# Optimization experiments

Measured on AMD Instinct MI355X. Metric: run time of the kernel, lower is better.

The kernel has to match this reference:

```python
import jax, jax.numpy as jnp
import numpy as np

EMBED_DIM = 32
HIDDEN_DIM = 16

def _xavier(key, fan_in, fan_out):
    limit = float(np.sqrt(6.0 / (fan_in + fan_out)))
    return jax.random.uniform(key, (fan_in, fan_out), jnp.float32, -limit, limit)

def setup_inputs() -> dict:
    key = jax.random.key(0)
    ks = jax.random.split(key, 7)
    N = 1_000_000
    H = jax.random.normal(ks[0], (N, EMBED_DIM), jnp.float32)
    TPL = jax.random.normal(ks[1], (1, 1), jnp.float32)
    # params (xavier-uniform weights, zero biases, matching torch init)
    Wv = _xavier(ks[2], EMBED_DIM, HIDDEN_DIM); bv = jnp.zeros((HIDDEN_DIM,), jnp.float32)
    Wu = _xavier(ks[3], EMBED_DIM, HIDDEN_DIM); bu = jnp.zeros((HIDDEN_DIM,), jnp.float32)
    Ww = _xavier(ks[4], HIDDEN_DIM, 1);        bw = jnp.zeros((1,), jnp.float32)
    W1 = _xavier(ks[5], EMBED_DIM + 1, HIDDEN_DIM); b1 = jnp.zeros((HIDDEN_DIM,), jnp.float32)
    W2 = _xavier(ks[6], HIDDEN_DIM, 1);        b2 = jnp.zeros((1,), jnp.float32)
    return {"H": H, "TPL": TPL, "Wv": Wv, "bv": bv, "Wu": Wu, "bu": bu,
            "Ww": Ww, "bw": bw, "W1": W1, "b1": b1, "W2": W2, "b2": b2}

def reference(H, TPL, Wv, bv, Wu, bu, Ww, bw, W1, b1, W2, b2):
    # Gated attention: V (tanh branch) * U (sigmoid branch); dropout off (eval mode)
    V = jnp.tanh(H @ Wv + bv)                       # (N, hid)
    U = jax.nn.sigmoid(H @ Wu + bu)                 # (N, hid)
    G = V * U                                       # (N, hid)
    A_raw = G @ Ww + bw                             # (N, 1)
    alpha = jax.nn.softmax(A_raw.T, axis=1)         # (1, N)
    B = alpha @ H                                   # (1, D) attention-pooled bag rep
    B_fused = jnp.concatenate([B, TPL], axis=1)     # (1, D+1)
    h = jax.nn.relu(B_fused @ W1 + b1)              # (1, hid)
    score = h @ W2 + b2                             # (1, 1)
    return (score, alpha)
```

## Files before the change

kernel.cpp:

```cpp
#include <hip/hip_runtime.h>

#define NBLK   1024
#define TPB    256
#define D      32
#define HID    16
#define CHUNK  16
#define STRIDE 36
#define NWAVES (NBLK * 4)

__global__ __launch_bounds__(TPB, 4)
void k1_logits(const float* __restrict__ H,
               const float* __restrict__ Wv, const float* __restrict__ bv,
               const float* __restrict__ Wu, const float* __restrict__ bu,
               const float* __restrict__ Ww, const float* __restrict__ bw,
               float* __restrict__ eout,
               float* __restrict__ partials,
               int N)
{
    __shared__ float lds[TPB / 64][CHUNK * STRIDE];
    __shared__ float red[TPB / 64][D + 1];

    const int tid  = threadIdx.x;
    const int wave = tid >> 6;
    const int lane = tid & 63;
    const int g    = lane >> 4;
    const int h    = lane & 15;

    float wv[D], wu[D];
    #pragma unroll
    for (int d = 0; d < D; ++d) {
        wv[d] = Wv[d * HID + h];
        wu[d] = Wu[d * HID + h];
    }
    const float bvh = bv[h], buh = bu[h], wwh = Ww[h], bw0 = bw[0];

    float s_acc = 0.0f, vec0 = 0.0f, vec1 = 0.0f;

    float* slice = lds[wave];
    const int nchunk = N / CHUNK;
    int c = blockIdx.x * (TPB / 64) + wave;

    float4 pre0, pre1;
    bool has = (c < nchunk);
    if (has) {
        const float4* src = reinterpret_cast<const float4*>(H + (size_t)c * CHUNK * D);
        pre0 = src[lane];
        pre1 = src[lane + 64];
    }

    while (has) {
        {
            const int f0 = lane,      r0i = f0 >> 3, q0 = f0 & 7;
            const int f1 = lane + 64, r1i = f1 >> 3, q1 = f1 & 7;
            *reinterpret_cast<float4*>(&slice[r0i * STRIDE + q0 * 4]) = pre0;
            *reinterpret_cast<float4*>(&slice[r1i * STRIDE + q1 * 4]) = pre1;
        }

        const int cn = c + NWAVES;
        const bool hn = (cn < nchunk);
        if (hn) {
            const float4* src = reinterpret_cast<const float4*>(H + (size_t)cn * CHUNK * D);
            pre0 = src[lane];
            pre1 = src[lane + 64];
        }

        #pragma unroll
        for (int s = 0; s < 4; ++s) {
            const int rr = s * 4 + g;
            const float* row = &slice[rr * STRIDE];

            float v = bvh, u = buh;
            #pragma unroll
            for (int q = 0; q < 8; ++q) {
                const float4 t4 = *reinterpret_cast<const float4*>(&row[q * 4]);
                v = fmaf(t4.x, wv[q * 4 + 0], v);  u = fmaf(t4.x, wu[q * 4 + 0], u);
                v = fmaf(t4.y, wv[q * 4 + 1], v);  u = fmaf(t4.y, wu[q * 4 + 1], u);
                v = fmaf(t4.z, wv[q * 4 + 2], v);  u = fmaf(t4.z, wu[q * 4 + 2], u);
                v = fmaf(t4.w, wv[q * 4 + 3], v);  u = fmaf(t4.w, wu[q * 4 + 3], u);
            }
            const float th = 1.0f - 2.0f / (__expf(2.0f * v) + 1.0f);
            const float sg = 1.0f / (1.0f + __expf(-u));
            float pa = th * sg * wwh;
            pa += __shfl_xor(pa, 1);
            pa += __shfl_xor(pa, 2);
            pa += __shfl_xor(pa, 4);
            pa += __shfl_xor(pa, 8);
            const float e = __expf(pa + bw0);
            if (h == 0) eout[c * CHUNK + rr] = e;
            s_acc += e;
            const float2 rp = *reinterpret_cast<const float2*>(&row[2 * h]);
            vec0 = fmaf(e, rp.x, vec0);
            vec1 = fmaf(e, rp.y, vec1);
        }
        c = cn;
        has = hn;
    }

    s_acc += __shfl_xor(s_acc, 16);  s_acc += __shfl_xor(s_acc, 32);
    vec0  += __shfl_xor(vec0, 16);   vec0  += __shfl_xor(vec0, 32);
    vec1  += __shfl_xor(vec1, 16);   vec1  += __shfl_xor(vec1, 32);

    if (lane == 0) red[wave][0] = s_acc;
    if (lane < 16) {
        red[wave][1 + 2 * h] = vec0;
        red[wave][2 + 2 * h] = vec1;
    }
    __syncthreads();
    if (tid < D + 1) {
        float p = red[0][tid] + red[1][tid] + red[2][tid] + red[3][tid];
        partials[(size_t)tid * NBLK + blockIdx.x] = p;
    }
}

__global__ __launch_bounds__(320)
void k2_reduce(const float* __restrict__ partials,
               const float* __restrict__ TPL,
               const float* __restrict__ W1, const float* __restrict__ b1,
               const float* __restrict__ W2, const float* __restrict__ b2,
               float* __restrict__ score_out,
               float* __restrict__ scalars)
{
    __shared__ double red[D + 1][8];
    __shared__ double tot[D + 1];
    const int t = threadIdx.x;

    if (t < (D + 1) * 8) {
        const int j = t >> 3, sl = t & 7;
        double acc = 0.0;
        for (int b = sl; b < NBLK; b += 8)
            acc += (double)partials[(size_t)j * NBLK + b];
        red[j][sl] = acc;
    }
    __syncthreads();
    if (t < D + 1) {
        double a = 0.0;
        #pragma unroll
        for (int k = 0; k < 8; ++k) a += red[t][k];
        tot[t] = a;
    }
    __syncthreads();
    if (t < HID) {
        const double S = tot[0];
        float hj = b1[t];
        #pragma unroll
        for (int k = 0; k < D; ++k)
            hj = fmaf((float)(tot[1 + k] / S), W1[k * HID + t], hj);
        hj = fmaf(TPL[0], W1[D * HID + t], hj);
        hj = fmaxf(hj, 0.0f);
        float pre = hj * W2[t];
        pre += __shfl_xor(pre, 1);
        pre += __shfl_xor(pre, 2);
        pre += __shfl_xor(pre, 4);
        pre += __shfl_xor(pre, 8);
        if (t == 0) {
            score_out[0] = pre + b2[0];
            scalars[0] = (float)(1.0 / S);
        }
    }
}

__global__ __launch_bounds__(TPB)
void k3_alpha(float* __restrict__ alpha, const float* __restrict__ scalars, int N)
{
    const int i = blockIdx.x * TPB + threadIdx.x;
    if (i < N) alpha[i] = alpha[i] * scalars[0];
}

extern "C" void kernel_launch(void* const* d_in, const int* in_sizes, int n_in,
                              void* d_out, int out_size, void* d_ws, size_t ws_size,
                              hipStream_t stream) {
    const float* H   = (const float*)d_in[0];
    const float* TPL = (const float*)d_in[1];
    const float* Wv  = (const float*)d_in[2];
    const float* bv  = (const float*)d_in[3];
    const float* Wu  = (const float*)d_in[4];
    const float* bu  = (const float*)d_in[5];
    const float* Ww  = (const float*)d_in[6];
    const float* bw  = (const float*)d_in[7];
    const float* W1  = (const float*)d_in[8];
    const float* b1  = (const float*)d_in[9];
    const float* W2  = (const float*)d_in[10];
    const float* b2  = (const float*)d_in[11];

    float* out = (float*)d_out;
    const int N = in_sizes[0] / D;

    float* ws       = (float*)d_ws;
    float* partials = ws;
    float* scalars  = ws + (size_t)(D + 1) * NBLK;

    k1_logits<<<NBLK, TPB, 0, stream>>>(H, Wv, bv, Wu, bu, Ww, bw,
                                        out + 1, partials, N);
    k2_reduce<<<1, 320, 0, stream>>>(partials, TPL, W1, b1, W2, b2, out, scalars);
    k3_alpha<<<(N + TPB - 1) / TPB, TPB, 0, stream>>>(out + 1, scalars, N);
}
```

Measured before the change: 236.4 us.

## Parallelize partial reduction, vectorize alpha scaling, spread logit stores, hoist prefetch

The single-block reduction kernel is replaced by a 33-block kernel where each block reduces one column of partials with wave shuffles in double precision. The score MLP moves into the alpha-normalization kernel, which now scales alpha with aligned float4 accesses (offset by 3 because the output is shifted by one float). In the main kernel, the prefetch of the next chunk is issued before the LDS store, and the per-row logit stores are spread over four lanes per group instead of one. The aim is to cut serial reduction latency and the store and launch overhead of the tail kernels, at the cost of extra registers for the double-buffered prefetch.

New measurement: 216.3 us. 1.09x faster.

```diff
diff --git a/kernel.cpp b/kernel.cpp
--- a/kernel.cpp
+++ b/kernel.cpp
@@ -49,6 +49,15 @@
     }
 
     while (has) {
+        const int cn = c + NWAVES;
+        const bool hn = (cn < nchunk);
+        float4 nxt0, nxt1;
+        if (hn) {
+            const float4* src = reinterpret_cast<const float4*>(H + (size_t)cn * CHUNK * D);
+            nxt0 = src[lane];
+            nxt1 = src[lane + 64];
+        }
+
         {
             const int f0 = lane,      r0i = f0 >> 3, q0 = f0 & 7;
             const int f1 = lane + 64, r1i = f1 >> 3, q1 = f1 & 7;
@@ -56,14 +65,7 @@
             *reinterpret_cast<float4*>(&slice[r1i * STRIDE + q1 * 4]) = pre1;
         }
 
-        const int cn = c + NWAVES;
-        const bool hn = (cn < nchunk);
-        if (hn) {
-            const float4* src = reinterpret_cast<const float4*>(H + (size_t)cn * CHUNK * D);
-            pre0 = src[lane];
-            pre1 = src[lane + 64];
-        }
-
+        float my_e = 0.0f;
         #pragma unroll
         for (int s = 0; s < 4; ++s) {
             const int rr = s * 4 + g;
@@ -86,12 +88,15 @@
             pa += __shfl_xor(pa, 4);
             pa += __shfl_xor(pa, 8);
             const float e = __expf(pa + bw0);
-            if (h == 0) eout[c * CHUNK + rr] = e;
+            if (h == s) my_e = e;
             s_acc += e;
             const float2 rp = *reinterpret_cast<const float2*>(&row[2 * h]);
             vec0 = fmaf(e, rp.x, vec0);
             vec1 = fmaf(e, rp.y, vec1);
         }
+        if (h < 4) eout[c * CHUNK + h * 4 + g] = my_e;
+
+        pre0 = nxt0; pre1 = nxt1;
         c = cn;
         has = hn;
     }
@@ -112,39 +117,53 @@
     }
 }
 
-__global__ __launch_bounds__(320)
-void k2_reduce(const float* __restrict__ partials,
-               const float* __restrict__ TPL,
-               const float* __restrict__ W1, const float* __restrict__ b1,
-               const float* __restrict__ W2, const float* __restrict__ b2,
-               float* __restrict__ score_out,
-               float* __restrict__ scalars)
+__global__ __launch_bounds__(TPB)
+void k2a_reduce(const float* __restrict__ partials,
+                double* __restrict__ tot,
+                float* __restrict__ scalars)
 {
-    __shared__ double red[D + 1][8];
-    __shared__ double tot[D + 1];
-    const int t = threadIdx.x;
-
-    if (t < (D + 1) * 8) {
-        const int j = t >> 3, sl = t & 7;
-        double acc = 0.0;
-        for (int b = sl; b < NBLK; b += 8)
-            acc += (double)partials[(size_t)j * NBLK + b];
-        red[j][sl] = acc;
-    }
+    const int j = blockIdx.x, t = threadIdx.x;
+    const float4 v = reinterpret_cast<const float4*>(partials + (size_t)j * NBLK)[t];
+    double a = (double)v.x + (double)v.y + (double)v.z + (double)v.w;
+    #pragma unroll
+    for (int m = 1; m <= 32; m <<= 1) a += __shfl_xor(a, m);
+    __shared__ double r[TPB / 64];
+    if ((t & 63) == 0) r[t >> 6] = a;
     __syncthreads();
-    if (t < D + 1) {
-        double a = 0.0;
-        #pragma unroll
-        for (int k = 0; k < 8; ++k) a += red[t][k];
-        tot[t] = a;
-    }
-    __syncthreads();
-    if (t < HID) {
-        const double S = tot[0];
+    if (t == 0) {
+        const double s = r[0] + r[1] + r[2] + r[3];
+        tot[j] = s;
+        if (j == 0) scalars[0] = (float)(1.0 / s);
+    }
+}
+
+__global__ __launch_bounds__(TPB)
+void k3_alpha(float* __restrict__ alpha,
+              const float* __restrict__ scalars,
+              const double* __restrict__ tot,
+              const float* __restrict__ TPL,
+              const float* __restrict__ W1, const float* __restrict__ b1,
+              const float* __restrict__ W2, const float* __restrict__ b2,
+              float* __restrict__ score_out, int N)
+{
+    const float invS = scalars[0];
+    const int i4 = blockIdx.x * TPB + threadIdx.x;
+    const int n4 = (N - 3) >> 2;
+    if (i4 < n4) {
+        float4* p = reinterpret_cast<float4*>(alpha + 3) + i4;
+        float4 v = *p;
+        v.x *= invS; v.y *= invS; v.z *= invS; v.w *= invS;
+        *p = v;
+    } else if (i4 == n4) {
+        alpha[0] *= invS; alpha[1] *= invS; alpha[2] *= invS;
+        for (int r = 3 + 4 * n4; r < N; ++r) alpha[r] *= invS;
+    }
+    if (blockIdx.x == 0 && threadIdx.x < HID) {
+        const int t = threadIdx.x;
         float hj = b1[t];
         #pragma unroll
         for (int k = 0; k < D; ++k)
-            hj = fmaf((float)(tot[1 + k] / S), W1[k * HID + t], hj);
+            hj = fmaf((float)(tot[1 + k] * (double)invS), W1[k * HID + t], hj);
         hj = fmaf(TPL[0], W1[D * HID + t], hj);
         hj = fmaxf(hj, 0.0f);
         float pre = hj * W2[t];
@@ -152,18 +171,8 @@
         pre += __shfl_xor(pre, 2);
         pre += __shfl_xor(pre, 4);
         pre += __shfl_xor(pre, 8);
-        if (t == 0) {
-            score_out[0] = pre + b2[0];
-            scalars[0] = (float)(1.0 / S);
-        }
-    }
-}
-
-__global__ __launch_bounds__(TPB)
-void k3_alpha(float* __restrict__ alpha, const float* __restrict__ scalars, int N)
-{
-    const int i = blockIdx.x * TPB + threadIdx.x;
-    if (i < N) alpha[i] = alpha[i] * scalars[0];
+        if (t == 0) score_out[0] = pre + b2[0];
+    }
 }
 
 extern "C" void kernel_launch(void* const* d_in, const int* in_sizes, int n_in,
@@ -185,12 +194,15 @@
     float* out = (float*)d_out;
     const int N = in_sizes[0] / D;
 
-    float* ws       = (float*)d_ws;
-    float* partials = ws;
-    float* scalars  = ws + (size_t)(D + 1) * NBLK;
+    float*  ws_f     = (float*)d_ws;
+    float*  partials = ws_f;
+    double* tot      = (double*)(ws_f + (size_t)(D + 1) * NBLK);
+    float*  scalars  = ws_f + (size_t)(D + 1) * NBLK + 2 * (D + 1) + 2;
 
     k1_logits<<<NBLK, TPB, 0, stream>>>(H, Wv, bv, Wu, bu, Ww, bw,
                                         out + 1, partials, N);
-    k2_reduce<<<1, 320, 0, stream>>>(partials, TPL, W1, b1, W2, b2, out, scalars);
-    k3_alpha<<<(N + TPB - 1) / TPB, TPB, 0, stream>>>(out + 1, scalars, N);
-}
+    k2a_reduce<<<D + 1, TPB, 0, stream>>>(partials, tot, scalars);
+    const int n4 = (N - 3) >> 2;
+    k3_alpha<<<(n4 + 1 + TPB - 1) / TPB, TPB, 0, stream>>>(out + 1, scalars, tot,
+                                                           TPL, W1, b1, W2, b2, out, N);
+}
```
